# Optimization experiments

Hardware: AMD Instinct MI355X
Metric: run time of the kernel (lower is better)

The kernel has to match this reference:

```python
import jax, jax.numpy as jnp
import numpy as np

E, N = 160000, 16000
NC = 8          # channels per degree (nc_in == nc_out)
MID = 32        # radial MLP hidden width
EDGE_DIM = 16   # n_dims_edge (graph.edata['w'] width)
PAIRS = [(0, 0), (0, 1), (1, 0), (1, 1)]


def _radial_mlp(x, w1, b1, w2, b2, w3, b3):
    # RadialFunc: Linear-BN-ReLU-Linear-BN-ReLU-Linear (BN is identity at eval defaults)
    h = jax.nn.relu(x @ w1 + b1)
    h = jax.nn.relu(h @ w2 + b2)
    return h @ w3 + b3


def setup_inputs():
    key = jax.random.key(0)
    ks = iter(jax.random.split(key, 64))
    inp = {}
    inp["feat_0"] = jax.random.normal(next(ks), (N, NC, 1), jnp.float32)
    inp["feat_1"] = jax.random.normal(next(ks), (N, NC, 3), jnp.float32)
    inp["w"] = jax.random.normal(next(ks), (E, EDGE_DIM), jnp.float32)
    inp["radial"] = jax.random.uniform(next(ks), (E, 1), jnp.float32)
    for di, do in PAIRS:
        nf = 2 * min(di, do) + 1
        inp[f"basis_{di}_{do}"] = jax.random.normal(next(ks), (E, 2 * do + 1, 2 * di + 1, nf), jnp.float32)
        inp[f"w1_{di}_{do}"] = jax.random.normal(next(ks), (EDGE_DIM + 1, MID), jnp.float32) / np.float32(np.sqrt(EDGE_DIM + 1))
        inp[f"b1_{di}_{do}"] = jnp.zeros((MID,), jnp.float32)
        inp[f"w2_{di}_{do}"] = jax.random.normal(next(ks), (MID, MID), jnp.float32) / np.float32(np.sqrt(MID))
        inp[f"b2_{di}_{do}"] = jnp.zeros((MID,), jnp.float32)
        inp[f"w3_{di}_{do}"] = jax.random.normal(next(ks), (MID, nf * NC * NC), jnp.float32) / np.float32(np.sqrt(MID))
        inp[f"b3_{di}_{do}"] = jnp.zeros((nf * NC * NC,), jnp.float32)
    inp["src_idx"] = jax.random.randint(next(ks), (E,), 0, N)
    return inp


def reference(feat_0, feat_1, w, radial,
              basis_0_0, basis_0_1, basis_1_0, basis_1_1,
              w1_0_0, b1_0_0, w2_0_0, b2_0_0, w3_0_0, b3_0_0,
              w1_0_1, b1_0_1, w2_0_1, b2_0_1, w3_0_1, b3_0_1,
              w1_1_0, b1_1_0, w2_1_0, b2_1_0, w3_1_0, b3_1_0,
              w1_1_1, b1_1_1, w2_1_1, b2_1_1, w3_1_1, b3_1_1,
              src_idx):
    feats = {0: feat_0, 1: feat_1}
    basis = {(0, 0): basis_0_0, (0, 1): basis_0_1, (1, 0): basis_1_0, (1, 1): basis_1_1}
    params = {(0, 0): (w1_0_0, b1_0_0, w2_0_0, b2_0_0, w3_0_0, b3_0_0),
              (0, 1): (w1_0_1, b1_0_1, w2_0_1, b2_0_1, w3_0_1, b3_0_1),
              (1, 0): (w1_1_0, b1_1_0, w2_1_0, b2_1_0, w3_1_0, b3_1_0),
              (1, 1): (w1_1_1, b1_1_1, w2_1_1, b2_1_1, w3_1_1, b3_1_1)}
    # edge_feats = cat(graph.edata['w'], radial)  -> [E, EDGE_DIM+1]
    ef = jnp.concatenate([w, radial], axis=-1)
    # per-edge gather of source node features: [E, NC, 2d+1]
    src = {d: feats[d][src_idx] for d in (0, 1)}
    outs = []
    for do in (0, 1):
        msg = 0.0
        for di in (0, 1):
            nf = 2 * min(di, do) + 1
            # PairwiseConv: R [E, nc_out, nc_in, nf]; kernel = sum_f R * basis
            R = _radial_mlp(ef, *params[(di, do)]).reshape(E, NC, NC, nf)
            # kernel_{e,o,p,i,q} = sum_f R_{e,o,i,f} basis_{e,p,q,f}; msg_{e,o,p} = kernel @ src
            msg = msg + jnp.einsum('eoif,epqf,eiq->eop', R, basis[(di, do)], src[di])
        outs.append(msg)  # [E, NC, 2*do+1]
    return tuple(outs)
```

## Files before the change

### kernel.cpp

```cpp
#include <hip/hip_runtime.h>

typedef unsigned int u32;
typedef _Float16 f16x8  __attribute__((ext_vector_type(8)));
typedef float    f32x16 __attribute__((ext_vector_type(16)));
typedef _Float16 v2h  __attribute__((ext_vector_type(2)));
typedef __fp16   v2fp __attribute__((ext_vector_type(2)));

#define E_TOT 160000
#define TPB   256
#define NBLK  1250
#define ASTR  20


#define MFMA(a,b,c) __builtin_amdgcn_mfma_f32_32x32x16_f16((a),(b),(c),0,0,0)

__device__ __forceinline__ u32 pkh(float a, float b){
  union { v2fp h; u32 x; } u;
  u.h = __builtin_amdgcn_cvt_pkrtz(a, b);
  return u.x;
}
__device__ __forceinline__ v2h asvh(u32 x){
  union { u32 x; v2h h; } u; u.x = x; return u.h;
}

struct WPtrs { const float* p[24]; };

__global__ __launch_bounds__(256) void prep_kernel(WPtrs S, u32* __restrict__ ws)
{
  const int t = blockIdx.x*256 + threadIdx.x;
  if (t >= 10496) return;
  float a = 0.f, b = 0.f;
  if (t < 10240){
    const int pair = (t < 6144) ? (t >> 11) : 3;
    const int rel  = t - ((pair < 3) ? (pair << 11) : 6144);
    const float* __restrict__ w1 = S.p[pair*6+0];
    const float* __restrict__ b1 = S.p[pair*6+1];
    const float* __restrict__ w2 = S.p[pair*6+2];
    const float* __restrict__ w3 = S.p[pair*6+4];
    const int N3  = (pair < 3) ? 8  : 24;
    const int NC3 = (pair < 3) ? 64 : 192;
    if (rel < 512){
      int o = rel >> 4, k0 = (rel & 15)*2;
      a = (k0   < 17) ? w1[k0*32 + o]     : ((k0   == 17) ? b1[o] : 0.f);
      b = (k0+1 < 17) ? w1[(k0+1)*32 + o] : ((k0+1 == 17) ? b1[o] : 0.f);
    } else if (rel < 1024){
      int j = rel - 512; int o = j >> 4, k0 = (j & 15)*2;
      a = w2[k0*32 + o]; b = w2[(k0+1)*32 + o];
    } else {
      int j = rel - 1024; int rp = j >> 4, k0 = (j & 15)*2;
      int col = (rp & 7)*N3 + (rp >> 3);
      a = w3[k0*NC3 + col]; b = w3[(k0+1)*NC3 + col];
    }
  } else {
    const int rel  = t - 10240;
    const int pair = (rel < 144) ? (rel / 48) : 3;
    const int r2   = rel - ((pair < 3) ? pair*48 : 144);
    const float* __restrict__ b2 = S.p[pair*6+3];
    const float* __restrict__ b3 = S.p[pair*6+5];
    const int N3 = (pair < 3) ? 8 : 24;
    if (r2 < 16){ a = b2[2*r2]; b = b2[2*r2+1]; }
    else {
      int r0 = (r2-16)*2, r1 = r0+1;
      a = b3[(r0 & 7)*N3 + (r0 >> 3)];
      b = b3[(r1 & 7)*N3 + (r1 >> 3)];
    }
  }
  ws[t] = pkh(a, b);
}

__device__ __forceinline__ f16x8 ldfrag(const u32* __restrict__ p){
  union { uint4 u; f16x8 h; } c;
  c.u = *(const uint4*)p;
  return c.h;
}
__device__ __forceinline__ f16x8 ldB(const u32* AS, int hi, int kk){
  union { uint4 u; f16x8 h; } c;
  c.u = *(const uint4*)(AS + 8*kk + 4*hi);
  return c.h;
}
__device__ __forceinline__ void packH(u32* AS, int hi, const f32x16& c){
  #pragma unroll
  for (int q = 0; q < 4; ++q){
    u32 ua = pkh(fmaxf(c[4*q+0],0.f), fmaxf(c[4*q+1],0.f));
    u32 ub = pkh(fmaxf(c[4*q+2],0.f), fmaxf(c[4*q+3],0.f));
    *(uint2*)(AS + 4*q + 2*hi) = make_uint2(ua, ub);
  }
}
__device__ __forceinline__ f32x16 ldbias(const u32* __restrict__ ws, int base, int m, int hi){
  f32x16 c;
  #pragma unroll
  for (int q = 0; q < 4; ++q){
    uint2 v = *(const uint2*)(ws + base + m*16 + 4*q + 2*hi);
    v2h lo = asvh(v.x), hh = asvh(v.y);
    c[4*q+0] = (float)lo[0]; c[4*q+1] = (float)lo[1];
    c[4*q+2] = (float)hh[0]; c[4*q+3] = (float)hh[1];
  }
  return c;
}

__device__ __forceinline__ void mlp12(const u32* __restrict__ ws, int pb, int b2base,
                                      int row, int hi, f16x8 bx0, f16x8 bx1, u32* AS)
{
  const u32* W = ws + pb + row*16 + hi*4;
  f32x16 c;
  #pragma unroll
  for (int i = 0; i < 16; ++i) c[i] = 0.f;
  c = MFMA(ldfrag(W),     bx0, c);
  c = MFMA(ldfrag(W + 8), bx1, c);
  packH(AS, hi, c);
  f16x8 h0 = ldB(AS, hi, 0), h1 = ldB(AS, hi, 1);
  f32x16 c2 = ldbias(ws, b2base, 0, hi);
  c2 = MFMA(ldfrag(W + 512),     h0, c2);
  c2 = MFMA(ldfrag(W + 512 + 8), h1, c2);
  packH(AS, hi, c2);
}

__device__ __forceinline__ void l3acc(const u32* __restrict__ ws, int w3base, int b3base,
                                      int row, int hi, const u32* AS,
                                      const float (&v)[8], float (&acc)[4])
{
  f16x8 h0 = ldB(AS, hi, 0), h1 = ldB(AS, hi, 1);
  #pragma unroll
  for (int m = 0; m < 2; ++m){
    f32x16 c3 = ldbias(ws, b3base, m, hi);
    const u32* W = ws + w3base + (m*32 + row)*16 + hi*4;
    c3 = MFMA(ldfrag(W),     h0, c3);
    c3 = MFMA(ldfrag(W + 8), h1, c3);
    #pragma unroll
    for (int r = 0; r < 16; ++r)
      acc[r & 3] = fmaf(c3[r], v[4*m + (r >> 2)], acc[r & 3]);
  }
}

__global__ __launch_bounds__(TPB, 2) void edge_kernel(
    const float* __restrict__ feat0, const float* __restrict__ feat1,
    const float* __restrict__ wE,    const float* __restrict__ radial,
    const float* __restrict__ b00,   const float* __restrict__ b01,
    const float* __restrict__ b10,   const float* __restrict__ b11,
    const int* __restrict__ src_idx, const u32* __restrict__ ws,
    float* __restrict__ out)
{
  __shared__ u32 XA[128 * ASTR];
  const int tid = threadIdx.x;
  const int w   = tid >> 6;
  const int hi  = (tid >> 5) & 1;
  const int row = tid & 31;
  const int e   = blockIdx.x*128 + w*32 + row;
  u32* AS = XA + (w*32 + row)*ASTR;
  const int idx = src_idx[e];

  f16x8 bx0, bx1;
  {
    const float4* wp = (const float4*)(wE + (size_t)e*16 + 8*hi);
    float4 x0 = wp[0], x1 = wp[1];
    union { uint4 u; f16x8 h; } cc;
    cc.u = make_uint4(pkh(x0.x,x0.y), pkh(x0.z,x0.w), pkh(x1.x,x1.y), pkh(x1.z,x1.w));
    bx0 = cc.h;
    cc.u = make_uint4(hi ? 0u : pkh(radial[e], 1.0f), 0u, 0u, 0u);
    bx1 = cc.h;
  }
  float f0v[8];
  {
    const float4* f = (const float4*)(feat0 + (size_t)idx*8);
    float4 u0 = f[0], u1 = f[1];
    f0v[0]=u0.x; f0v[1]=u0.y; f0v[2]=u0.z; f0v[3]=u0.w;
    f0v[4]=u1.x; f0v[5]=u1.y; f0v[6]=u1.z; f0v[7]=u1.w;
  }
  float f1v[24];
  {
    const float4* f = (const float4*)(feat1 + (size_t)idx*24);
    #pragma unroll
    for (int j = 0; j < 6; ++j){
      float4 v = f[j];
      f1v[4*j+0]=v.x; f1v[4*j+1]=v.y; f1v[4*j+2]=v.z; f1v[4*j+3]=v.w;
    }
  }
  const float bB = b00[e];
  float B10v[3], B01v[3];
  #pragma unroll
  for (int q = 0; q < 3; ++q){
    B10v[q] = b10[(size_t)e*3 + q];
    B01v[q] = b01[(size_t)e*3 + q];
  }
  float Uv[8];
  #pragma unroll
  for (int i = 0; i < 8; ++i)
    Uv[i] = fmaf(B10v[0], f1v[3*i], fmaf(B10v[1], f1v[3*i+1], B10v[2]*f1v[3*i+2]));

  float mA[4] = {0.f, 0.f, 0.f, 0.f};
  mlp12(ws,    0, 10240, row, hi, bx0, bx1, AS);
  l3acc(ws, 1024, 10256, row, hi, AS, f0v, mA);
  #pragma unroll
  for (int j = 0; j < 4; ++j) mA[j] *= bB;
  mlp12(ws, 2048, 10288, row, hi, bx0, bx1, AS);
  l3acc(ws, 2048+1024, 10304, row, hi, AS, Uv, mA);
  *(float4*)(out + (size_t)e*8 + 4*hi) = make_float4(mA[0], mA[1], mA[2], mA[3]);

  float t01m[4] = {0.f, 0.f, 0.f, 0.f};
  mlp12(ws, 4096, 10336, row, hi, bx0, bx1, AS);
  l3acc(ws, 4096+1024, 10352, row, hi, AS, f0v, t01m);
  mlp12(ws, 6144, 10384, row, hi, bx0, bx1, AS);
  float Bv[27];
  {
    const float* __restrict__ bp = b11 + (size_t)e*27;
    #pragma unroll
    for (int j = 0; j < 27; ++j) Bv[j] = bp[j];
  }
  float m1[12];
  #pragma unroll
  for (int o2 = 0; o2 < 4; ++o2)
    #pragma unroll
    for (int p = 0; p < 3; ++p)
      m1[o2*3+p] = t01m[o2] * B01v[p];
  {
    f16x8 h0 = ldB(AS, hi, 0), h1 = ldB(AS, hi, 1);
    #pragma unroll
    for (int m = 0; m < 6; ++m){
      f32x16 c3 = ldbias(ws, 10400, m, hi);
      const u32* W = ws + 7168 + (m*32 + row)*16 + hi*4;
      c3 = MFMA(ldfrag(W),     h0, c3);
      c3 = MFMA(ldfrag(W + 8), h1, c3);
      float C1[4][3];
      #pragma unroll
      for (int t2 = 0; t2 < 4; ++t2){
        const int ifp = 4*m + t2;
        const int ii = ifp / 3, ff = ifp - 3*ii;
        #pragma unroll
        for (int p = 0; p < 3; ++p)
          C1[t2][p] = fmaf(Bv[p*9 + 0 + ff], f1v[ii*3 + 0],
                      fmaf(Bv[p*9 + 3 + ff], f1v[ii*3 + 1],
                           Bv[p*9 + 6 + ff] * f1v[ii*3 + 2]));
      }
      #pragma unroll
      for (int r = 0; r < 16; ++r)
        #pragma unroll
        for (int p = 0; p < 3; ++p)
          m1[(r & 3)*3 + p] = fmaf(c3[r], C1[r >> 2][p], m1[(r & 3)*3 + p]);
    }
  }
  float* o1 = out + (size_t)E_TOT*8 + (size_t)e*24 + 12*hi;
  ((float4*)o1)[0] = make_float4(m1[0], m1[1], m1[2],  m1[3]);
  ((float4*)o1)[1] = make_float4(m1[4], m1[5], m1[6],  m1[7]);
  ((float4*)o1)[2] = make_float4(m1[8], m1[9], m1[10], m1[11]);
}

extern "C" void kernel_launch(void* const* d_in, const int* in_sizes, int n_in,
                              void* d_out, int out_size, void* d_ws, size_t ws_size,
                              hipStream_t stream)
{
  const float* feat0 = (const float*)d_in[0];
  const float* feat1 = (const float*)d_in[1];
  const float* wE    = (const float*)d_in[2];
  const float* rad   = (const float*)d_in[3];
  const float* b00   = (const float*)d_in[4];
  const float* b01   = (const float*)d_in[11];
  const float* b10   = (const float*)d_in[18];
  const float* b11   = (const float*)d_in[25];
  const int* sidx    = (const int*)d_in[32];
  u32* ws            = (u32*)d_ws;

  const int base[4] = {5, 19, 12, 26};
  WPtrs S;
  for (int p = 0; p < 4; ++p)
    for (int k = 0; k < 6; ++k)
      S.p[p*6 + k] = (const float*)d_in[base[p] + k];

  prep_kernel<<<41, 256, 0, stream>>>(S, ws);
  edge_kernel<<<NBLK, TPB, 0, stream>>>(feat0, feat1, wE, rad, b00, b01, b10, b11,
                                        sidx, ws, (float*)d_out);
}
```

Before: 170.5 us.

## Keep MLP hidden activations in registers via permuted weights; process two edge tiles per wave

Permutes the rows of the first- and second-layer weights and biases during prep so that the MFMA accumulator layout can be repacked straight into the B-operand fragment of the next layer. This drops the LDS round-trip (shared array, stores and reloads) between MLP layers. Each wave now handles two 32-edge tiles, so weight fragments are loaded once and reused for both, and the grid is halved. The cost is more registers per thread, which may hurt occupancy or cause spills.

```diff
diff --git a/kernel.cpp b/kernel.cpp
--- a/kernel.cpp
+++ b/kernel.cpp
@@ -8,8 +8,7 @@
 
 #define E_TOT 160000
 #define TPB   256
-#define NBLK  1250
-#define ASTR  20
+#define NBLK  625
 
 
 #define MFMA(a,b,c) __builtin_amdgcn_mfma_f32_32x32x16_f16((a),(b),(c),0,0,0)
@@ -21,6 +20,9 @@
 }
 __device__ __forceinline__ v2h asvh(u32 x){
   union { u32 x; v2h h; } u; u.x = x; return u.h;
+}
+__device__ __forceinline__ int MU(int p){
+  return ((((p >> 2) ^ (p >> 3)) & 1) ? (p ^ 12) : p);
 }
 
 struct WPtrs { const float* p[24]; };
@@ -40,11 +42,11 @@
     const int N3  = (pair < 3) ? 8  : 24;
     const int NC3 = (pair < 3) ? 64 : 192;
     if (rel < 512){
-      int o = rel >> 4, k0 = (rel & 15)*2;
+      int o = MU(rel >> 4), k0 = (rel & 15)*2;
       a = (k0   < 17) ? w1[k0*32 + o]     : ((k0   == 17) ? b1[o] : 0.f);
       b = (k0+1 < 17) ? w1[(k0+1)*32 + o] : ((k0+1 == 17) ? b1[o] : 0.f);
     } else if (rel < 1024){
-      int j = rel - 512; int o = j >> 4, k0 = (j & 15)*2;
+      int j = rel - 512; int o = MU(j >> 4), k0 = (j & 15)*2;
       a = w2[k0*32 + o]; b = w2[(k0+1)*32 + o];
     } else {
       int j = rel - 1024; int rp = j >> 4, k0 = (j & 15)*2;
@@ -58,8 +60,9 @@
     const float* __restrict__ b2 = S.p[pair*6+3];
     const float* __restrict__ b3 = S.p[pair*6+5];
     const int N3 = (pair < 3) ? 8 : 24;
-    if (r2 < 16){ a = b2[2*r2]; b = b2[2*r2+1]; }
-    else {
+    if (r2 < 16){
+      a = b2[MU(2*r2)]; b = b2[MU(2*r2+1)];
+    } else {
       int r0 = (r2-16)*2, r1 = r0+1;
       a = b3[(r0 & 7)*N3 + (r0 >> 3)];
       b = b3[(r1 & 7)*N3 + (r1 >> 3)];
@@ -72,19 +75,6 @@
   union { uint4 u; f16x8 h; } c;
   c.u = *(const uint4*)p;
   return c.h;
-}
-__device__ __forceinline__ f16x8 ldB(const u32* AS, int hi, int kk){
-  union { uint4 u; f16x8 h; } c;
-  c.u = *(const uint4*)(AS + 8*kk + 4*hi);
-  return c.h;
-}
-__device__ __forceinline__ void packH(u32* AS, int hi, const f32x16& c){
-  #pragma unroll
-  for (int q = 0; q < 4; ++q){
-    u32 ua = pkh(fmaxf(c[4*q+0],0.f), fmaxf(c[4*q+1],0.f));
-    u32 ub = pkh(fmaxf(c[4*q+2],0.f), fmaxf(c[4*q+3],0.f));
-    *(uint2*)(AS + 4*q + 2*hi) = make_uint2(ua, ub);
-  }
 }
 __device__ __forceinline__ f32x16 ldbias(const u32* __restrict__ ws, int base, int m, int hi){
   f32x16 c;
@@ -97,39 +87,129 @@
   }
   return c;
 }
-
-__device__ __forceinline__ void mlp12(const u32* __restrict__ ws, int pb, int b2base,
-                                      int row, int hi, f16x8 bx0, f16x8 bx1, u32* AS)
+__device__ __forceinline__ void packfrag(const f32x16& c, f16x8& k0, f16x8& k1){
+  union { uint4 u; f16x8 h; } a, b;
+  a.u = make_uint4(pkh(fmaxf(c[0], 0.f),  fmaxf(c[1], 0.f)),
+                   pkh(fmaxf(c[2], 0.f),  fmaxf(c[3], 0.f)),
+                   pkh(fmaxf(c[4], 0.f),  fmaxf(c[5], 0.f)),
+                   pkh(fmaxf(c[6], 0.f),  fmaxf(c[7], 0.f)));
+  b.u = make_uint4(pkh(fmaxf(c[8], 0.f),  fmaxf(c[9], 0.f)),
+                   pkh(fmaxf(c[10],0.f),  fmaxf(c[11],0.f)),
+                   pkh(fmaxf(c[12],0.f),  fmaxf(c[13],0.f)),
+                   pkh(fmaxf(c[14],0.f),  fmaxf(c[15],0.f)));
+  k0 = a.h; k1 = b.h;
+}
+
+__device__ __forceinline__ void mlp12_2(const u32* __restrict__ ws, int pb, int b2base,
+                                        int row, int hi,
+                                        const f16x8 (&bx0)[2], const f16x8 (&bx1)[2],
+                                        f16x8 (&h0)[2], f16x8 (&h1)[2])
 {
   const u32* W = ws + pb + row*16 + hi*4;
-  f32x16 c;
-  #pragma unroll
-  for (int i = 0; i < 16; ++i) c[i] = 0.f;
-  c = MFMA(ldfrag(W),     bx0, c);
-  c = MFMA(ldfrag(W + 8), bx1, c);
-  packH(AS, hi, c);
-  f16x8 h0 = ldB(AS, hi, 0), h1 = ldB(AS, hi, 1);
-  f32x16 c2 = ldbias(ws, b2base, 0, hi);
-  c2 = MFMA(ldfrag(W + 512),     h0, c2);
-  c2 = MFMA(ldfrag(W + 512 + 8), h1, c2);
-  packH(AS, hi, c2);
-}
-
-__device__ __forceinline__ void l3acc(const u32* __restrict__ ws, int w3base, int b3base,
-                                      int row, int hi, const u32* AS,
-                                      const float (&v)[8], float (&acc)[4])
-{
-  f16x8 h0 = ldB(AS, hi, 0), h1 = ldB(AS, hi, 1);
+  f16x8 wa = ldfrag(W), wb = ldfrag(W + 8);
+  f16x8 g0[2], g1[2];
+  #pragma unroll
+  for (int t = 0; t < 2; ++t){
+    f32x16 z;
+    #pragma unroll
+    for (int i = 0; i < 16; ++i) z[i] = 0.f;
+    z = MFMA(wa, bx0[t], z);
+    z = MFMA(wb, bx1[t], z);
+    packfrag(z, g0[t], g1[t]);
+  }
+  f16x8 w2a = ldfrag(W + 512), w2b = ldfrag(W + 520);
+  f32x16 bias = ldbias(ws, b2base, 0, hi);
+  #pragma unroll
+  for (int t = 0; t < 2; ++t){
+    f32x16 z = bias;
+    z = MFMA(w2a, g0[t], z);
+    z = MFMA(w2b, g1[t], z);
+    packfrag(z, h0[t], h1[t]);
+  }
+}
+
+__device__ __forceinline__ void l3acc_2(const u32* __restrict__ ws, int w3base, int b3base,
+                                        int row, int hi,
+                                        const f16x8 (&h0)[2], const f16x8 (&h1)[2],
+                                        const float (&v)[2][8], float (&acc)[2][4])
+{
   #pragma unroll
   for (int m = 0; m < 2; ++m){
-    f32x16 c3 = ldbias(ws, b3base, m, hi);
+    f32x16 bias = ldbias(ws, b3base, m, hi);
     const u32* W = ws + w3base + (m*32 + row)*16 + hi*4;
+    f16x8 wa = ldfrag(W), wb = ldfrag(W + 8);
+    #pragma unroll
+    for (int t = 0; t < 2; ++t){
+      f32x16 c3 = bias;
+      c3 = MFMA(wa, h0[t], c3);
+      c3 = MFMA(wb, h1[t], c3);
+      #pragma unroll
+      for (int r = 0; r < 16; ++r)
+        acc[t][r & 3] = fmaf(c3[r], v[t][4*m + (r >> 2)], acc[t][r & 3]);
+    }
+  }
+}
+
+__device__ __forceinline__ void epiB(const u32* __restrict__ ws,
+                                     const float* __restrict__ feat1,
+                                     const float* __restrict__ b01,
+                                     const float* __restrict__ b11,
+                                     float* __restrict__ out,
+                                     int e, int idx, int row, int hi,
+                                     const float (&t01m)[4],
+                                     f16x8 h0, f16x8 h1)
+{
+  float f1v[24];
+  {
+    const float4* f = (const float4*)(feat1 + (size_t)idx*24);
+    #pragma unroll
+    for (int j = 0; j < 6; ++j){
+      float4 v = f[j];
+      f1v[4*j+0]=v.x; f1v[4*j+1]=v.y; f1v[4*j+2]=v.z; f1v[4*j+3]=v.w;
+    }
+  }
+  float Bv[27];
+  {
+    const float* __restrict__ bp = b11 + (size_t)e*27;
+    #pragma unroll
+    for (int j = 0; j < 27; ++j) Bv[j] = bp[j];
+  }
+  float B01q[3];
+  #pragma unroll
+  for (int q = 0; q < 3; ++q) B01q[q] = b01[(size_t)e*3 + q];
+  float m1[12];
+  #pragma unroll
+  for (int o2 = 0; o2 < 4; ++o2)
+    #pragma unroll
+    for (int p = 0; p < 3; ++p)
+      m1[o2*3+p] = t01m[o2] * B01q[p];
+  #pragma unroll
+  for (int m = 0; m < 6; ++m){
+    f32x16 c3 = ldbias(ws, 10400, m, hi);
+    const u32* W = ws + 7168 + (m*32 + row)*16 + hi*4;
     c3 = MFMA(ldfrag(W),     h0, c3);
     c3 = MFMA(ldfrag(W + 8), h1, c3);
+    float C1[4][3];
+    #pragma unroll
+    for (int t2 = 0; t2 < 4; ++t2){
+      const int ifp = 4*m + t2;
+      const int ii = ifp / 3, ff = ifp - 3*ii;
+      #pragma unroll
+      for (int p = 0; p < 3; ++p)
+        C1[t2][p] = fmaf(Bv[p*9 + 0 + ff], f1v[ii*3 + 0],
+                    fmaf(Bv[p*9 + 3 + ff], f1v[ii*3 + 1],
+                         Bv[p*9 + 6 + ff] * f1v[ii*3 + 2]));
+    }
     #pragma unroll
     for (int r = 0; r < 16; ++r)
-      acc[r & 3] = fmaf(c3[r], v[4*m + (r >> 2)], acc[r & 3]);
-  }
+      #pragma unroll
+      for (int p = 0; p < 3; ++p)
+        m1[(r & 3)*3 + p] = fmaf(c3[r], C1[r >> 2][p], m1[(r & 3)*3 + p]);
+  }
+  float* o1 = out + (size_t)E_TOT*8 + (size_t)e*24 + 12*hi;
+  ((float4*)o1)[0] = make_float4(m1[0], m1[1], m1[2],  m1[3]);
+  ((float4*)o1)[1] = make_float4(m1[4], m1[5], m1[6],  m1[7]);
+  ((float4*)o1)[2] = make_float4(m1[8], m1[9], m1[10], m1[11]);
 }
 
 __global__ __launch_bounds__(TPB, 2) void edge_kernel(
@@ -140,108 +220,88 @@
     const int* __restrict__ src_idx, const u32* __restrict__ ws,
     float* __restrict__ out)
 {
-  __shared__ u32 XA[128 * ASTR];
   const int tid = threadIdx.x;
   const int w   = tid >> 6;
   const int hi  = (tid >> 5) & 1;
   const int row = tid & 31;
-  const int e   = blockIdx.x*128 + w*32 + row;
-  u32* AS = XA + (w*32 + row)*ASTR;
-  const int idx = src_idx[e];
-
-  f16x8 bx0, bx1;
-  {
+  const int e0  = blockIdx.x*256 + w*64 + row;
+
+  int idx[2];
+  f16x8 bx0[2], bx1[2];
+  #pragma unroll
+  for (int t = 0; t < 2; ++t){
+    const int e = e0 + 32*t;
+    idx[t] = src_idx[e];
     const float4* wp = (const float4*)(wE + (size_t)e*16 + 8*hi);
     float4 x0 = wp[0], x1 = wp[1];
     union { uint4 u; f16x8 h; } cc;
     cc.u = make_uint4(pkh(x0.x,x0.y), pkh(x0.z,x0.w), pkh(x1.x,x1.y), pkh(x1.z,x1.w));
-    bx0 = cc.h;
+    bx0[t] = cc.h;
     cc.u = make_uint4(hi ? 0u : pkh(radial[e], 1.0f), 0u, 0u, 0u);
-    bx1 = cc.h;
-  }
-  float f0v[8];
-  {
-    const float4* f = (const float4*)(feat0 + (size_t)idx*8);
+    bx1[t] = cc.h;
+  }
+  float f0v[2][8];
+  #pragma unroll
+  for (int t = 0; t < 2; ++t){
+    const float4* f = (const float4*)(feat0 + (size_t)idx[t]*8);
     float4 u0 = f[0], u1 = f[1];
-    f0v[0]=u0.x; f0v[1]=u0.y; f0v[2]=u0.z; f0v[3]=u0.w;
-    f0v[4]=u1.x; f0v[5]=u1.y; f0v[6]=u1.z; f0v[7]=u1.w;
-  }
-  float f1v[24];
-  {
-    const float4* f = (const float4*)(feat1 + (size_t)idx*24);
+    f0v[t][0]=u0.x; f0v[t][1]=u0.y; f0v[t][2]=u0.z; f0v[t][3]=u0.w;
+    f0v[t][4]=u1.x; f0v[t][5]=u1.y; f0v[t][6]=u1.z; f0v[t][7]=u1.w;
+  }
+  float Uv[2][8], bB[2];
+  #pragma unroll
+  for (int t = 0; t < 2; ++t){
+    const int e = e0 + 32*t;
+    bB[t] = b00[e];
+    float B10q[3];
+    #pragma unroll
+    for (int q = 0; q < 3; ++q) B10q[q] = b10[(size_t)e*3 + q];
+    float f1t[24];
+    const float4* f = (const float4*)(feat1 + (size_t)idx[t]*24);
     #pragma unroll
     for (int j = 0; j < 6; ++j){
       float4 v = f[j];
-      f1v[4*j+0]=v.x; f1v[4*j+1]=v.y; f1v[4*j+2]=v.z; f1v[4*j+3]=v.w;
-    }
-  }
-  const float bB = b00[e];
-  float B10v[3], B01v[3];
-  #pragma unroll
-  for (int q = 0; q < 3; ++q){
-    B10v[q] = b10[(size_t)e*3 + q];
-    B01v[q] = b01[(size_t)e*3 + q];
-  }
-  float Uv[8];
-  #pragma unroll
-  for (int i = 0; i < 8; ++i)
-    Uv[i] = fmaf(B10v[0], f1v[3*i], fmaf(B10v[1], f1v[3*i+1], B10v[2]*f1v[3*i+2]));
-
-  float mA[4] = {0.f, 0.f, 0.f, 0.f};
-  mlp12(ws,    0, 10240, row, hi, bx0, bx1, AS);
-  l3acc(ws, 1024, 10256, row, hi, AS, f0v, mA);
-  #pragma unroll
-  for (int j = 0; j < 4; ++j) mA[j] *= bB;
-  mlp12(ws, 2048, 10288, row, hi, bx0, bx1, AS);
-  l3acc(ws, 2048+1024, 10304, row, hi, AS, Uv, mA);
-  *(float4*)(out + (size_t)e*8 + 4*hi) = make_float4(mA[0], mA[1], mA[2], mA[3]);
-
-  float t01m[4] = {0.f, 0.f, 0.f, 0.f};
-  mlp12(ws, 4096, 10336, row, hi, bx0, bx1, AS);
-  l3acc(ws, 4096+1024, 10352, row, hi, AS, f0v, t01m);
-  mlp12(ws, 6144, 10384, row, hi, bx0, bx1, AS);
-  float Bv[27];
+      f1t[4*j+0]=v.x; f1t[4*j+1]=v.y; f1t[4*j+2]=v.z; f1t[4*j+3]=v.w;
+    }
+    #pragma unroll
+    for (int i = 0; i < 8; ++i)
+      Uv[t][i] = fmaf(B10q[0], f1t[3*i], fmaf(B10q[1], f1t[3*i+1], B10q[2]*f1t[3*i+2]));
+  }
+
+  f16x8 h0[2], h1[2];
+  float mA[2][4];
+  #pragma unroll
+  for (int t = 0; t < 2; ++t)
+    #pragma unroll
+    for (int j = 0; j < 4; ++j) mA[t][j] = 0.f;
+  mlp12_2(ws,    0, 10240, row, hi, bx0, bx1, h0, h1);
+  l3acc_2(ws, 1024, 10256, row, hi, h0, h1, f0v, mA);
+  #pragma unroll
+  for (int t = 0; t < 2; ++t)
+    #pragma unroll
+    for (int j = 0; j < 4; ++j) mA[t][j] *= bB[t];
+  mlp12_2(ws, 2048, 10288, row, hi, bx0, bx1, h0, h1);
+  l3acc_2(ws, 3072, 10304, row, hi, h0, h1, Uv, mA);
+  #pragma unroll
+  for (int t = 0; t < 2; ++t){
+    const int e = e0 + 32*t;
+    *(float4*)(out + (size_t)e*8 + 4*hi) = make_float4(mA[t][0], mA[t][1], mA[t][2], mA[t][3]);
+  }
+
+  float t01m[2][4];
+  #pragma unroll
+  for (int t = 0; t < 2; ++t)
+    #pragma unroll
+    for (int j = 0; j < 4; ++j) t01m[t][j] = 0.f;
+  mlp12_2(ws, 4096, 10336, row, hi, bx0, bx1, h0, h1);
+  l3acc_2(ws, 5120, 10352, row, hi, h0, h1, f0v, t01m);
+  mlp12_2(ws, 6144, 10384, row, hi, bx0, bx1, h0, h1);
   {
-    const float* __restrict__ bp = b11 + (size_t)e*27;
-    #pragma unroll
-    for (int j = 0; j < 27; ++j) Bv[j] = bp[j];
-  }
-  float m1[12];
-  #pragma unroll
-  for (int o2 = 0; o2 < 4; ++o2)
-    #pragma unroll
-    for (int p = 0; p < 3; ++p)
-      m1[o2*3+p] = t01m[o2] * B01v[p];
-  {
-    f16x8 h0 = ldB(AS, hi, 0), h1 = ldB(AS, hi, 1);
-    #pragma unroll
-    for (int m = 0; m < 6; ++m){
-      f32x16 c3 = ldbias(ws, 10400, m, hi);
-      const u32* W = ws + 7168 + (m*32 + row)*16 + hi*4;
-      c3 = MFMA(ldfrag(W),     h0, c3);
-      c3 = MFMA(ldfrag(W + 8), h1, c3);
-      float C1[4][3];
-      #pragma unroll
-      for (int t2 = 0; t2 < 4; ++t2){
-        const int ifp = 4*m + t2;
-        const int ii = ifp / 3, ff = ifp - 3*ii;
-        #pragma unroll
-        for (int p = 0; p < 3; ++p)
-          C1[t2][p] = fmaf(Bv[p*9 + 0 + ff], f1v[ii*3 + 0],
-                      fmaf(Bv[p*9 + 3 + ff], f1v[ii*3 + 1],
-                           Bv[p*9 + 6 + ff] * f1v[ii*3 + 2]));
-      }
-      #pragma unroll
-      for (int r = 0; r < 16; ++r)
-        #pragma unroll
-        for (int p = 0; p < 3; ++p)
-          m1[(r & 3)*3 + p] = fmaf(c3[r], C1[r >> 2][p], m1[(r & 3)*3 + p]);
-    }
-  }
-  float* o1 = out + (size_t)E_TOT*8 + (size_t)e*24 + 12*hi;
-  ((float4*)o1)[0] = make_float4(m1[0], m1[1], m1[2],  m1[3]);
-  ((float4*)o1)[1] = make_float4(m1[4], m1[5], m1[6],  m1[7]);
-  ((float4*)o1)[2] = make_float4(m1[8], m1[9], m1[10], m1[11]);
+    float t0[4] = {t01m[0][0], t01m[0][1], t01m[0][2], t01m[0][3]};
+    epiB(ws, feat1, b01, b11, out, e0,      idx[0], row, hi, t0, h0[0], h1[0]);
+    float t1[4] = {t01m[1][0], t01m[1][1], t01m[1][2], t01m[1][3]};
+    epiB(ws, feat1, b01, b11, out, e0 + 32, idx[1], row, hi, t1, h0[1], h1[1]);
+  }
 }
 
 extern "C" void kernel_launch(void* const* d_in, const int* in_sizes, int n_in,
```

Measured after the change: 224.9 us. 1.32x slower.
